# Kernel tuning notes

Hardware: AMD Instinct MI355X
Metric: run time of the kernel (lower is better)

The kernel has to match this reference:

```python
import jax, jax.numpy as jnp
import numpy as np

N_NODES = 10000
N_EDGES = 160000
MAX_K = 8
IN_NF = 64
HID = 64
ED = 16
HEADS = 4
NVEC = 5

def _mlp2_silu(x, w1, b1, w2, b2):
    # Linear -> SiLU -> Linear -> SiLU
    return jax.nn.silu(jax.nn.silu(x @ w1 + b1) @ w2 + b2)

def _mlp_out(x, w1, b1, w2, b2):
    # Linear -> SiLU -> Linear
    return jax.nn.silu(x @ w1 + b1) @ w2 + b2

def _segment_mean(data, ids, n):
    s = jax.ops.segment_sum(data, ids, num_segments=n)
    c = jax.ops.segment_sum(jnp.ones_like(data), ids, num_segments=n)
    return s / jnp.maximum(c, 1.0)

def setup_inputs() -> dict:
    key = jax.random.key(0)
    ks = jax.random.split(key, 48)
    p = lambda k, shape: jax.random.normal(k, shape, dtype=jnp.float32) * 0.05
    inp = {
        "h": jax.random.normal(ks[0], (N_NODES, IN_NF), dtype=jnp.float32),
        "coord": jax.random.normal(ks[1], (N_NODES, 3), dtype=jnp.float32),
        "edges": jax.random.randint(ks[2], (2, N_EDGES), 0, N_NODES),
        "nvecs": jax.random.normal(ks[3], (N_NODES, NVEC, 3), dtype=jnp.float32),
        "edge_attr": jax.random.normal(ks[4], (N_EDGES, ED), dtype=jnp.float32),
        "node_attr": jax.random.normal(ks[5], (N_NODES, HID), dtype=jnp.float32),
        "init_coord": jax.random.normal(ks[6], (N_NODES, 3), dtype=jnp.float32),
    }
    kidx = jax.random.randint(ks[7], (N_EDGES, 2, MAX_K), 0, N_EDGES)
    red = jax.random.uniform(ks[8], (N_EDGES, MAX_K)) < 0.2
    inp["klist"] = jnp.where(red[:, None, :], -1, kidx)
    chem_in = 2 * IN_NF + 2 * HID + ED
    pos_in = NVEC + 15 + ED  # edge_coords_nf(20) + edges_in_d
    inp.update({
        "w_chem1": p(ks[9], (chem_in, HID)), "b_chem1": jnp.zeros((HID,), jnp.float32),
        "w_chem2": p(ks[10], (HID, HID)), "b_chem2": jnp.zeros((HID,), jnp.float32),
        "w_pos1": p(ks[11], (pos_in, HID)), "b_pos1": jnp.zeros((HID,), jnp.float32),
        "w_pos2": p(ks[12], (HID, HID)), "b_pos2": jnp.zeros((HID,), jnp.float32),
        "w_sh": p(ks[13], (HID, HID)), "b_sh": jnp.zeros((HID,), jnp.float32),
        "w_att": p(ks[14], (HID, 1)), "b_att": jnp.zeros((1,), jnp.float32),
        "wq": p(ks[15], (HEADS, HID, HID)),
        "wk": p(ks[16], (HEADS, HID, HID)),
        "wv": p(ks[17], (HEADS, HID, HID)),
        "wb": p(ks[18], (HEADS, HID)),
        "wg": p(ks[19], (HEADS, HID, HID)), "bg": jnp.zeros((HEADS, HID), jnp.float32),
        "w_out": p(ks[20], (HEADS * HID, HID)), "b_out": jnp.zeros((HID,), jnp.float32),
        "wu1": p(ks[21], (HID, HID)), "bu1": jnp.zeros((HID,), jnp.float32),
        "wu2": p(ks[22], (HID, 1)), "bu2": jnp.zeros((1,), jnp.float32),
        "wx1": p(ks[23], (HID, HID)), "bx1": jnp.zeros((HID,), jnp.float32),
        "wx2": p(ks[24], (HID, 1)), "bx2": jnp.zeros((1,), jnp.float32),
        "wh1": p(ks[25], (2 * HID + IN_NF, HID)), "bh1": jnp.zeros((HID,), jnp.float32),
        "wh2": p(ks[26], (HID, HID)), "bh2": jnp.zeros((HID,), jnp.float32),
    })
    return inp

def reference(h, coord, edges, nvecs, edge_attr, node_attr, init_coord, klist,
              w_chem1, b_chem1, w_chem2, b_chem2, w_pos1, b_pos1, w_pos2, b_pos2,
              w_sh, b_sh, w_att, b_att, wq, wk, wv, wb, wg, bg, w_out, b_out,
              wu1, bu1, wu2, bu2, wx1, bx1, wx2, bx2, wh1, bh1, wh2, bh2):
    row, col = edges[0], edges[1]
    # radial features + normalized coordinate differences
    cd = coord[row] - coord[col]
    cd = cd / (jnp.linalg.norm(cd, axis=-1, keepdims=True) + 1e-8)
    init_radial = jnp.sum(cd ** 2, axis=1, keepdims=True)                 # (E, 1)
    radial = jnp.exp(init_radial * (-0.5 / 2.25 ** jnp.arange(15.0)))     # (E, 15)
    nprod = jnp.sum(nvecs[row] * nvecs[col], axis=-1)                     # (E, NVEC)
    chem = _mlp2_silu(jnp.concatenate([h[row], h[col], node_attr[row], node_attr[col], edge_attr], axis=1),
                      w_chem1, b_chem1, w_chem2, b_chem2)
    pos = _mlp2_silu(jnp.concatenate([nprod, radial, edge_attr], axis=1),
                     w_pos1, b_pos1, w_pos2, b_pos2)
    z = jax.nn.silu(chem @ w_sh + b_sh) * pos
    z = z * jax.nn.sigmoid(z @ w_att + b_att)
    # triangle k-NN attention over edges
    idx_i2k, idx_j2k = klist[:, 0], klist[:, 1]                           # (E, K)
    red = idx_i2k == -1
    heads = []
    for hd in range(HEADS):
        q = z @ wq[hd]; k_ = z @ wk[hd]; v = z @ wv[hd]; b = z @ wb[hd]
        g = jax.nn.sigmoid(z @ wg[hd] + bg[hd])
        tri_k = jnp.where(red[:, :, None], 0.0, k_[idx_i2k])              # (E, K, HID)
        tri_b = jnp.where(red, 0.0, b[idx_j2k])                           # (E, K)
        tri_v = v[idx_i2k]                                                # (E, K, HID)
        alpha = jnp.einsum('ed,ekd->ek', q, tri_k) / np.sqrt(HID) + tri_b
        alpha = jax.nn.softmax(jnp.where(red, -10000.0, alpha), axis=1)
        heads.append(g * jnp.einsum('ek,ekd->ed', alpha, tri_v))
    m = jnp.concatenate(heads, axis=-1) @ w_out + b_out
    # equivariant coordinate update
    ita = 0.2
    x_trans = cd * (_mlp_out(chem, wu1, bu1, wu2, bu2) * _mlp_out(pos, wx1, bx1, wx2, bx2))
    x_agg = _segment_mean(x_trans, row, N_NODES)
    coord_new = ita * init_coord + (1.0 - ita) * coord + x_agg
    m_agg = _segment_mean(m, row, N_NODES)
    h_new = h + _mlp_out(jnp.concatenate([h, node_attr, m_agg], axis=-1), wh1, bh1, wh2, bh2)
    return (h_new, coord_new)
```

## Files before the change

### kernel.cpp

```cpp
#include <hip/hip_runtime.h>
#include <math.h>

#define NE 160000
#define NN 10000

#define DEV __device__ __forceinline__

typedef float v2f __attribute__((ext_vector_type(2)));
typedef __attribute__((ext_vector_type(8))) short bf16x8;
typedef __attribute__((ext_vector_type(4))) float f32x4;

DEV float fsilu(float x) { return x / (1.0f + __expf(-x)); }
DEV float fsig(float x)  { return 1.0f / (1.0f + __expf(-x)); }

DEV unsigned pack2(float a, float b) {
  unsigned ua = __float_as_uint(a); ua += 0x7FFFu + ((ua >> 16) & 1u);
  unsigned ub = __float_as_uint(b); ub += 0x7FFFu + ((ub >> 16) & 1u);
  return (ua >> 16) | (ub & 0xFFFF0000u);
}

DEV unsigned packf8_4(float a, float b, float c, float d) {
  int r = __builtin_amdgcn_cvt_pk_fp8_f32(a, b, 0, false);
  r = __builtin_amdgcn_cvt_pk_fp8_f32(c, d, r, true);
  return (unsigned)r;
}
template<bool HI>
DEV v2f up2(unsigned u) { return __builtin_amdgcn_cvt_pk_f32_fp8((int)u, HI); }

DEV float dot16(uint4 u, const float* q, float d) {
  v2f f;
  f = up2<false>(u.x); d = fmaf(f.x, q[0],  d); d = fmaf(f.y, q[1],  d);
  f = up2<true >(u.x); d = fmaf(f.x, q[2],  d); d = fmaf(f.y, q[3],  d);
  f = up2<false>(u.y); d = fmaf(f.x, q[4],  d); d = fmaf(f.y, q[5],  d);
  f = up2<true >(u.y); d = fmaf(f.x, q[6],  d); d = fmaf(f.y, q[7],  d);
  f = up2<false>(u.z); d = fmaf(f.x, q[8],  d); d = fmaf(f.y, q[9],  d);
  f = up2<true >(u.z); d = fmaf(f.x, q[10], d); d = fmaf(f.y, q[11], d);
  f = up2<false>(u.w); d = fmaf(f.x, q[12], d); d = fmaf(f.y, q[13], d);
  f = up2<true >(u.w); d = fmaf(f.x, q[14], d); d = fmaf(f.y, q[15], d);
  return d;
}
DEV void acc16(uint4 u, float pk, float* o) {
  v2f f;
  f = up2<false>(u.x); o[0]  = fmaf(pk, f.x, o[0]);  o[1]  = fmaf(pk, f.y, o[1]);
  f = up2<true >(u.x); o[2]  = fmaf(pk, f.x, o[2]);  o[3]  = fmaf(pk, f.y, o[3]);
  f = up2<false>(u.y); o[4]  = fmaf(pk, f.x, o[4]);  o[5]  = fmaf(pk, f.y, o[5]);
  f = up2<true >(u.y); o[6]  = fmaf(pk, f.x, o[6]);  o[7]  = fmaf(pk, f.y, o[7]);
  f = up2<false>(u.z); o[8]  = fmaf(pk, f.x, o[8]);  o[9]  = fmaf(pk, f.y, o[9]);
  f = up2<true >(u.z); o[10] = fmaf(pk, f.x, o[10]); o[11] = fmaf(pk, f.y, o[11]);
  f = up2<false>(u.w); o[12] = fmaf(pk, f.x, o[12]); o[13] = fmaf(pk, f.y, o[13]);
  f = up2<true >(u.w); o[14] = fmaf(pk, f.x, o[14]); o[15] = fmaf(pk, f.y, o[15]);
}

DEV void ldrow16(const unsigned* __restrict__ p, unsigned (&r)[16]) {
#pragma unroll
  for (int t = 0; t < 4; ++t) {
    uint4 u = ((const uint4*)p)[t];
    r[4*t] = u.x; r[4*t+1] = u.y; r[4*t+2] = u.z; r[4*t+3] = u.w;
  }
}
DEV void unpackf8(const unsigned (&p)[16], float (&o)[64]) {
#pragma unroll
  for (int t = 0; t < 16; ++t) {
    v2f f0 = up2<false>(p[t]);
    v2f f1 = up2<true >(p[t]);
    o[4*t+0] = f0.x; o[4*t+1] = f0.y; o[4*t+2] = f1.x; o[4*t+3] = f1.y;
  }
}
DEV void store32(float* dst, const float (&a)[32]) {
#pragma unroll
  for (int j = 0; j < 32; j += 4)
    *(float4*)(dst + j) = make_float4(a[j], a[j+1], a[j+2], a[j+3]);
}

DEV bf16x8 packrow8(const float* __restrict__ p) {
  float4 a = *(const float4*)p;
  float4 b = *(const float4*)(p + 4);
  uint4 u = make_uint4(pack2(a.x, a.y), pack2(a.z, a.w),
                       pack2(b.x, b.y), pack2(b.z, b.w));
  return __builtin_bit_cast(bf16x8, u);
}

DEV void mm4(const unsigned short* __restrict__ wm, int er, int q,
             const bf16x8 (&bfr)[2], f32x4 (&acc)[4]) {
#pragma unroll
  for (int nf = 0; nf < 4; ++nf) {
    const unsigned short* ar = wm + (size_t)(nf * 16 + er) * 64 + q * 8;
    const bf16x8 a0 = *(const bf16x8*)ar;
    const bf16x8 a1 = *(const bf16x8*)(ar + 32);
    acc[nf] = __builtin_amdgcn_mfma_f32_16x16x32_bf16(a0, bfr[0], acc[nf], 0, 0, 0);
    acc[nf] = __builtin_amdgcn_mfma_f32_16x16x32_bf16(a1, bfr[1], acc[nf], 0, 0, 0);
  }
}

__global__ void __launch_bounds__(256)
k_count(const int* __restrict__ edges, int* __restrict__ icnt) {
  int e = blockIdx.x * 256 + threadIdx.x;
  if (e < NE) atomicAdd(&icnt[edges[e]], 1);
}

__global__ void __launch_bounds__(256)
k_scan(const int* __restrict__ icnt, int* __restrict__ ioffs) {
  __shared__ int part[256];
  const int t = threadIdx.x;
  const int base = t * 40;
  int loc[40];
  int s = 0;
#pragma unroll
  for (int i = 0; i < 40; ++i) {
    int idx = base + i;
    int v = (idx < NN) ? icnt[idx] : 0;
    loc[i] = v; s += v;
  }
  part[t] = s;
  __syncthreads();
  for (int off = 1; off < 256; off <<= 1) {
    int v = (t >= off) ? part[t - off] : 0;
    __syncthreads();
    part[t] += v;
    __syncthreads();
  }
  int run = (t == 0) ? 0 : part[t - 1];
#pragma unroll
  for (int i = 0; i < 40; ++i) {
    int idx = base + i;
    if (idx < NN) { ioffs[idx] = run; run += loc[i]; }
  }
  if (t == 255) ioffs[NN] = NE;
}

__global__ void __launch_bounds__(256)
k_fill(const int* __restrict__ edges, const int* __restrict__ ioffs,
       int* __restrict__ icur, int* __restrict__ eidx) {
  int e = blockIdx.x * 256 + threadIdx.x;
  if (e >= NE) return;
  int r = edges[e];
  int p = atomicAdd(&icur[r], 1);
  eidx[ioffs[r] + p] = e;
}

__global__ void __launch_bounds__(256)
k_chem1m(const float* __restrict__ h, const float* __restrict__ na,
         const float* __restrict__ ea, const int* __restrict__ edges,
         const unsigned short* __restrict__ wtb, const float* __restrict__ b1,
         float* __restrict__ act1c) {
  const int lane = threadIdx.x & 63;
  const int wid  = threadIdx.x >> 6;
  const int er   = lane & 15;
  const int q    = lane >> 4;
  const int e    = blockIdx.x * 64 + wid * 16 + er;
  const int r = edges[e], c = edges[NE + e];

  const f32x4 zero = {0.f, 0.f, 0.f, 0.f};
  f32x4 acc[4] = {zero, zero, zero, zero};
  bf16x8 f[2];
  const float* xr;
  xr = h  + (size_t)r * 64; f[0] = packrow8(xr + q * 8); f[1] = packrow8(xr + 32 + q * 8);
  mm4(wtb + (size_t)29 * 4096, er, q, f, acc);
  xr = h  + (size_t)c * 64; f[0] = packrow8(xr + q * 8); f[1] = packrow8(xr + 32 + q * 8);
  mm4(wtb + (size_t)30 * 4096, er, q, f, acc);
  xr = na + (size_t)r * 64; f[0] = packrow8(xr + q * 8); f[1] = packrow8(xr + 32 + q * 8);
  mm4(wtb + (size_t)31 * 4096, er, q, f, acc);
  xr = na + (size_t)c * 64; f[0] = packrow8(xr + q * 8); f[1] = packrow8(xr + 32 + q * 8);
  mm4(wtb + (size_t)32 * 4096, er, q, f, acc);
  {
    bf16x8 ef;
    if (q < 2) ef = packrow8(ea + (size_t)e * 16 + q * 8);
    else { uint4 z4 = make_uint4(0, 0, 0, 0); ef = __builtin_bit_cast(bf16x8, z4); }
    const unsigned short* wm = wtb + (size_t)33 * 4096;
#pragma unroll
    for (int nf = 0; nf < 4; ++nf) {
      const bf16x8 a0 = *(const bf16x8*)(wm + (size_t)(nf * 16 + er) * 64 + q * 8);
      acc[nf] = __builtin_amdgcn_mfma_f32_16x16x32_bf16(a0, ef, acc[nf], 0, 0, 0);
    }
  }
#pragma unroll
  for (int nf = 0; nf < 4; ++nf) {
    const float4 b4 = *(const float4*)(b1 + nf * 16 + q * 4);
    *(float4*)(act1c + (size_t)e * 64 + nf * 16 + q * 4) =
        make_float4(fsilu(acc[nf].x + b4.x), fsilu(acc[nf].y + b4.y),
                    fsilu(acc[nf].z + b4.z), fsilu(acc[nf].w + b4.w));
  }
}

__global__ void __launch_bounds__(256)
k_pos1(const float* __restrict__ coord, const float* __restrict__ nv,
       const float* __restrict__ ea, const int* __restrict__ edges,
       const float* __restrict__ w1, const float* __restrict__ b1,
       float* __restrict__ act1p) {
  const int e = blockIdx.x * 256 + threadIdx.x;
  const int co = blockIdx.y * 32;
  const int r = edges[e], c = edges[NE + e];

  float dx = coord[r * 3 + 0] - coord[c * 3 + 0];
  float dy = coord[r * 3 + 1] - coord[c * 3 + 1];
  float dz = coord[r * 3 + 2] - coord[c * 3 + 2];
  float nrm = sqrtf(dx * dx + dy * dy + dz * dz);
  float inv = 1.0f / (nrm + 1e-8f);
  dx *= inv; dy *= inv; dz *= inv;
  float ir = dx * dx + dy * dy + dz * dz;

  float in[36];
#pragma unroll
  for (int v = 0; v < 5; ++v) {
    float s = 0.f;
#pragma unroll
    for (int d = 0; d < 3; ++d)
      s += nv[(size_t)r * 15 + v * 3 + d] * nv[(size_t)c * 15 + v * 3 + d];
    in[v] = s;
  }
  {
    float cexp = -0.5f;
#pragma unroll
    for (int k = 0; k < 15; ++k) { in[5 + k] = __expf(ir * cexp); cexp *= (1.0f / 2.25f); }
  }
#pragma unroll
  for (int k = 0; k < 16; k += 4) {
    float4 e4 = *(const float4*)(ea + (size_t)e * 16 + k);
    in[20 + k] = e4.x; in[21 + k] = e4.y; in[22 + k] = e4.z; in[23 + k] = e4.w;
  }

  float acc[32];
#pragma unroll
  for (int j = 0; j < 32; ++j) acc[j] = b1[co + j];
#pragma unroll
  for (int k = 0; k < 36; ++k) {
    const float x = in[k];
    const float* wr = w1 + (size_t)k * 64 + co;
#pragma unroll
    for (int j = 0; j < 32; ++j) acc[j] = fmaf(x, wr[j], acc[j]);
  }
#pragma unroll
  for (int j = 0; j < 32; ++j) acc[j] = fsilu(acc[j]);
  store32(act1p + (size_t)e * 64 + co, acc);
}

__global__ void __launch_bounds__(256)
k_wprep(const float* __restrict__ wk, const float* __restrict__ wv,
        const float* __restrict__ wq, const float* __restrict__ wg,
        const float* __restrict__ wsh, const float* __restrict__ wu1,
        const float* __restrict__ wx1, const float* __restrict__ wout,
        const float* __restrict__ wh1, const float* __restrict__ wh2,
        const float* __restrict__ w2c, const float* __restrict__ w2p,
        const float* __restrict__ wc1,
        unsigned short* __restrict__ wtb) {
  const int m = blockIdx.x;
  const float* src;
  bool pad16 = false, permk = false;
  if (m < 16) {
    const int hd = m >> 2, which = m & 3;
    src = ((which == 0) ? wk : (which == 1) ? wv : (which == 2) ? wq : wg)
          + (size_t)hd * 4096;
  } else if (m < 19) {
    src = (m == 16) ? wsh : (m == 17) ? wu1 : wx1;
  } else if (m < 23) {
    src = wout + (size_t)(m - 19) * 4096;
    permk = true;
  } else if (m < 26) {
    src = wh1 + (size_t)(m - 23) * 4096;
  } else if (m == 26) {
    src = wh2;
  } else if (m == 27) {
    src = w2c;
  } else if (m == 28) {
    src = w2p;
  } else if (m < 33) {
    src = wc1 + (size_t)(m - 29) * 4096;
  } else {
    src = wc1 + (size_t)4 * 4096;
    pad16 = true;
  }
  const int t = threadIdx.x;
#pragma unroll
  for (int i = 0; i < 16; ++i) {
    int idx = t * 16 + i;
    int n = idx >> 6, kk = idx & 63;
    int kr = permk ? (((kk >> 2) & 3) * 16 + (kk >> 4) * 4 + (kk & 3)) : kk;
    float v = (pad16 && kr >= 16) ? 0.f : src[kr * 64 + n];
    unsigned u = __float_as_uint(v);
    u += 0x7FFFu + ((u >> 16) & 1u);
    wtb[(size_t)m * 4096 + idx] = (unsigned short)(u >> 16);
  }
}

__global__ void __launch_bounds__(256)
k_l2s(const float* __restrict__ coord, const int* __restrict__ edges,
      const float* __restrict__ act1c, const float* __restrict__ act1p,
      const unsigned short* __restrict__ wtb,
      const float* __restrict__ b2c, const float* __restrict__ b2p,
      const float* __restrict__ bsh,
      const float* __restrict__ watt, const float* __restrict__ batt,
      const float* __restrict__ bu1, const float* __restrict__ wu2,
      const float* __restrict__ bu2,
      const float* __restrict__ bx1, const float* __restrict__ wx2,
      const float* __restrict__ bx2,
      const float* __restrict__ wb,
      unsigned* __restrict__ zb, float* __restrict__ be,
      float* __restrict__ x_sum, float* __restrict__ cntf) {
  __shared__ float ltc[4][16][68];
  __shared__ float ltp[4][16][68];
  const int lane = threadIdx.x & 63;
  const int wid  = threadIdx.x >> 6;
  const int er   = lane & 15;
  const int q    = lane >> 4;
  const int e    = blockIdx.x * 64 + wid * 16 + er;

  const f32x4 zero = {0.f, 0.f, 0.f, 0.f};
  bf16x8 f[2];

  {
    const float* xr = act1c + (size_t)e * 64;
    f[0] = packrow8(xr + q * 8); f[1] = packrow8(xr + 32 + q * 8);
  }
  f32x4 cD[4] = {zero, zero, zero, zero};
  mm4(wtb + (size_t)27 * 4096, er, q, f, cD);
#pragma unroll
  for (int nf = 0; nf < 4; ++nf) {
    const float4 bc = *(const float4*)(b2c + nf * 16 + q * 4);
    *(float4*)&ltc[wid][er][nf * 16 + q * 4] =
        make_float4(fsilu(cD[nf].x + bc.x), fsilu(cD[nf].y + bc.y),
                    fsilu(cD[nf].z + bc.z), fsilu(cD[nf].w + bc.w));
  }
  {
    const float* xr = act1p + (size_t)e * 64;
    f[0] = packrow8(xr + q * 8); f[1] = packrow8(xr + 32 + q * 8);
  }
  f32x4 pD[4] = {zero, zero, zero, zero};
  mm4(wtb + (size_t)28 * 4096, er, q, f, pD);
  float pv[16];
#pragma unroll
  for (int nf = 0; nf < 4; ++nf) {
    const float4 bp = *(const float4*)(b2p + nf * 16 + q * 4);
    pv[4*nf+0] = fsilu(pD[nf].x + bp.x); pv[4*nf+1] = fsilu(pD[nf].y + bp.y);
    pv[4*nf+2] = fsilu(pD[nf].z + bp.z); pv[4*nf+3] = fsilu(pD[nf].w + bp.w);
    *(float4*)&ltp[wid][er][nf * 16 + q * 4] =
        make_float4(pv[4*nf+0], pv[4*nf+1], pv[4*nf+2], pv[4*nf+3]);
  }
  bf16x8 cf[2], pf[2];
  cf[0] = packrow8(&ltc[wid][er][q * 8]); cf[1] = packrow8(&ltc[wid][er][32 + q * 8]);
  pf[0] = packrow8(&ltp[wid][er][q * 8]); pf[1] = packrow8(&ltp[wid][er][32 + q * 8]);

  float z[16];
  {
    f32x4 acc[4] = {zero, zero, zero, zero};
    mm4(wtb + (size_t)16 * 4096, er, q, cf, acc);
#pragma unroll
    for (int nf = 0; nf < 4; ++nf) {
      const float4 b4 = *(const float4*)(bsh + nf * 16 + q * 4);
      z[4*nf+0] = fsilu(acc[nf].x + b4.x) * pv[4*nf+0];
      z[4*nf+1] = fsilu(acc[nf].y + b4.y) * pv[4*nf+1];
      z[4*nf+2] = fsilu(acc[nf].z + b4.z) * pv[4*nf+2];
      z[4*nf+3] = fsilu(acc[nf].w + b4.w) * pv[4*nf+3];
    }
  }
  {
    float ap = 0.f;
#pragma unroll
    for (int nf = 0; nf < 4; ++nf)
#pragma unroll
      for (int r = 0; r < 4; ++r)
        ap = fmaf(z[4*nf+r], watt[nf * 16 + q * 4 + r], ap);
    ap += __shfl_xor(ap, 16);
    ap += __shfl_xor(ap, 32);
    const float sg = fsig(ap + batt[0]);
#pragma unroll
    for (int j = 0; j < 16; ++j) z[j] *= sg;
  }
  {
    unsigned* zrow = zb + (size_t)e * 32 + q * 2;
#pragma unroll
    for (int nf = 0; nf < 4; ++nf) {
      uint2 w = make_uint2(pack2(z[4*nf+0], z[4*nf+1]), pack2(z[4*nf+2], z[4*nf+3]));
      *(uint2*)(zrow + nf * 8) = w;
    }
  }
  {
    float bb[4];
#pragma unroll
    for (int hd = 0; hd < 4; ++hd) {
      float b = 0.f;
#pragma unroll
      for (int nf = 0; nf < 4; ++nf)
#pragma unroll
        for (int r = 0; r < 4; ++r)
          b = fmaf(z[4*nf+r], wb[hd * 64 + nf * 16 + q * 4 + r], b);
      b += __shfl_xor(b, 16);
      b += __shfl_xor(b, 32);
      bb[hd] = b;
    }
    if (q == 0)
      *(float4*)(be + (size_t)e * 4) = make_float4(bb[0], bb[1], bb[2], bb[3]);
  }
  float u;
  {
    f32x4 acc[4] = {zero, zero, zero, zero};
    mm4(wtb + (size_t)17 * 4096, er, q, cf, acc);
    float up = 0.f;
#pragma unroll
    for (int nf = 0; nf < 4; ++nf) {
      const float4 b4 = *(const float4*)(bu1 + nf * 16 + q * 4);
      const float4 w4 = *(const float4*)(wu2 + nf * 16 + q * 4);
      up = fmaf(fsilu(acc[nf].x + b4.x), w4.x, up);
      up = fmaf(fsilu(acc[nf].y + b4.y), w4.y, up);
      up = fmaf(fsilu(acc[nf].z + b4.z), w4.z, up);
      up = fmaf(fsilu(acc[nf].w + b4.w), w4.w, up);
    }
    up += __shfl_xor(up, 16);
    up += __shfl_xor(up, 32);
    u = up + bu2[0];
  }
  float xs;
  {
    f32x4 acc[4] = {zero, zero, zero, zero};
    mm4(wtb + (size_t)18 * 4096, er, q, pf, acc);
    float xp = 0.f;
#pragma unroll
    for (int nf = 0; nf < 4; ++nf) {
      const float4 b4 = *(const float4*)(bx1 + nf * 16 + q * 4);
      const float4 w4 = *(const float4*)(wx2 + nf * 16 + q * 4);
      xp = fmaf(fsilu(acc[nf].x + b4.x), w4.x, xp);
      xp = fmaf(fsilu(acc[nf].y + b4.y), w4.y, xp);
      xp = fmaf(fsilu(acc[nf].z + b4.z), w4.z, xp);
      xp = fmaf(fsilu(acc[nf].w + b4.w), w4.w, xp);
    }
    xp += __shfl_xor(xp, 16);
    xp += __shfl_xor(xp, 32);
    xs = xp + bx2[0];
  }

  if (q == 0) {
    const int r = edges[e], c = edges[NE + e];
    float dx = coord[r * 3 + 0] - coord[c * 3 + 0];
    float dy = coord[r * 3 + 1] - coord[c * 3 + 1];
    float dz = coord[r * 3 + 2] - coord[c * 3 + 2];
    float nrm = sqrtf(dx * dx + dy * dy + dz * dz);
    float inv = 1.0f / (nrm + 1e-8f);
    float t = u * xs;
    atomicAdd(&x_sum[r * 3 + 0], dx * inv * t);
    atomicAdd(&x_sum[r * 3 + 1], dy * inv * t);
    atomicAdd(&x_sum[r * 3 + 2], dz * inv * t);
    atomicAdd(&cntf[r], 1.0f);
  }
}

__global__ void __launch_bounds__(256)
k_projm(const unsigned* __restrict__ zb, const unsigned short* __restrict__ wtb,
        const float* __restrict__ bg,
        unsigned* __restrict__ ksep, unsigned* __restrict__ vsep,
        unsigned* __restrict__ qho, unsigned* __restrict__ gf8) {
  const int lane = threadIdx.x & 63;
  const int wid  = threadIdx.x >> 6;
  const int er   = lane & 15;
  const int q    = lane >> 4;
  const int e0   = blockIdx.x * 128 + wid * 32 + er;

  bf16x8 zf[2][2];
#pragma unroll
  for (int et = 0; et < 2; ++et) {
    const unsigned* zrow = zb + (size_t)(e0 + et * 16) * 32;
    zf[et][0] = __builtin_bit_cast(bf16x8, *(const uint4*)(zrow + q * 4));
    zf[et][1] = __builtin_bit_cast(bf16x8, *(const uint4*)(zrow + 16 + q * 4));
  }

  const f32x4 zero = {0.f, 0.f, 0.f, 0.f};
#pragma unroll 1
  for (int m = 0; m < 16; ++m) {
    const unsigned short* wm = wtb + (size_t)m * 4096;
    f32x4 acc[2][4];
#pragma unroll
    for (int et = 0; et < 2; ++et)
#pragma unroll
      for (int nf = 0; nf < 4; ++nf) acc[et][nf] = zero;
#pragma unroll
    for (int nf = 0; nf < 4; ++nf) {
      const unsigned short* ar = wm + (size_t)(nf * 16 + er) * 64 + q * 8;
      const bf16x8 a0 = *(const bf16x8*)ar;
      const bf16x8 a1 = *(const bf16x8*)(ar + 32);
#pragma unroll
      for (int et = 0; et < 2; ++et) {
        acc[et][nf] = __builtin_amdgcn_mfma_f32_16x16x32_bf16(a0, zf[et][0], acc[et][nf], 0, 0, 0);
        acc[et][nf] = __builtin_amdgcn_mfma_f32_16x16x32_bf16(a1, zf[et][1], acc[et][nf], 0, 0, 0);
      }
    }
    const int hd = m >> 2, which = m & 3;
#pragma unroll
    for (int et = 0; et < 2; ++et) {
      const size_t rec = (size_t)(e0 + et * 16) * 4 + hd;
      unsigned* dst = (which == 0) ? (ksep + rec * 16)
                    : (which == 1) ? (vsep + rec * 16)
                    : (which == 2) ? (qho + rec * 16)
                                   : (gf8 + rec * 16);
      unsigned pk[4];
      if (which == 3) {
#pragma unroll
        for (int nf = 0; nf < 4; ++nf) {
          const float4 b4 = *(const float4*)(bg + hd * 64 + nf * 16 + q * 4);
          pk[nf] = packf8_4(fsig(acc[et][nf].x + b4.x), fsig(acc[et][nf].y + b4.y),
                            fsig(acc[et][nf].z + b4.z), fsig(acc[et][nf].w + b4.w));
        }
      } else {
#pragma unroll
        for (int nf = 0; nf < 4; ++nf)
          pk[nf] = packf8_4(acc[et][nf].x, acc[et][nf].y,
                            acc[et][nf].z, acc[et][nf].w);
      }
      *(uint4*)(dst + q * 4) = make_uint4(pk[0], pk[1], pk[2], pk[3]);
    }
  }
}

__global__ void __launch_bounds__(256)
k_attn(unsigned* __restrict__ qho, unsigned* __restrict__ gf8,
       const unsigned* __restrict__ ksep, const unsigned* __restrict__ vsep,
       const float* __restrict__ be, const int* __restrict__ klist) {
  const int t = blockIdx.x * 256 + threadIdx.x;
  const int e = t >> 2, hd = t & 3;

  float q[64];
  {
    unsigned qp[16];
    ldrow16(qho + (size_t)t * 16, qp);
    unpackf8(qp, q);
  }

  int i2[8], j2[8];
#pragma unroll
  for (int kn = 0; kn < 8; ++kn) {
    i2[kn] = klist[(size_t)e * 16 + kn];
    j2[kn] = klist[(size_t)e * 16 + 8 + kn];
  }
  float bv[8];
#pragma unroll
  for (int kn = 0; kn < 8; ++kn)
    bv[kn] = be[(size_t)((i2[kn] < 0) ? 0 : j2[kn]) * 4 + hd];

  const uint4* k4 = (const uint4*)ksep;
  float alpha[8];
#pragma unroll 2
  for (int kn = 0; kn < 8; ++kn) {
    if (i2[kn] < 0) { alpha[kn] = -10000.0f; continue; }
    const uint4* kr = k4 + ((size_t)i2[kn] * 4 + hd) * 4;
    uint4 u0 = kr[0], u1 = kr[1], u2 = kr[2], u3 = kr[3];
    float d = 0.f;
    d = dot16(u0, q,      d);
    d = dot16(u1, q + 16, d);
    d = dot16(u2, q + 32, d);
    d = dot16(u3, q + 48, d);
    alpha[kn] = d * 0.125f + bv[kn];
  }
  float mx = alpha[0];
#pragma unroll
  for (int kn = 1; kn < 8; ++kn) mx = fmaxf(mx, alpha[kn]);
  float p[8], s = 0.f;
#pragma unroll
  for (int kn = 0; kn < 8; ++kn) { p[kn] = __expf(alpha[kn] - mx); s += p[kn]; }
  float is = 1.0f / s;
#pragma unroll
  for (int kn = 0; kn < 8; ++kn) p[kn] *= is;

  float ov[64];
#pragma unroll
  for (int j = 0; j < 64; ++j) ov[j] = 0.f;
  const uint4* v4 = (const uint4*)vsep;
#pragma unroll 2
  for (int kn = 0; kn < 8; ++kn) {
    int vi = (i2[kn] < 0) ? (NE - 1) : i2[kn];
    const uint4* vr = v4 + ((size_t)vi * 4 + hd) * 4;
    uint4 u0 = vr[0], u1 = vr[1], u2 = vr[2], u3 = vr[3];
    const float pk = p[kn];
    acc16(u0, pk, ov +  0);
    acc16(u1, pk, ov + 16);
    acc16(u2, pk, ov + 32);
    acc16(u3, pk, ov + 48);
  }
  {
    unsigned gp[16];
    ldrow16(gf8 + (size_t)t * 16, gp);
    float g[64];
    unpackf8(gp, g);
#pragma unroll
    for (int j = 0; j < 64; ++j) ov[j] *= g[j];
  }
  {
    unsigned* qr = qho + (size_t)t * 16;
    unsigned* gr = gf8 + (size_t)t * 16;
#pragma unroll
    for (int t2 = 0; t2 < 2; ++t2) {
      ((uint4*)qr)[t2] = make_uint4(pack2(ov[8*t2+0],  ov[8*t2+1]),  pack2(ov[8*t2+2],  ov[8*t2+3]),
                                    pack2(ov[8*t2+4],  ov[8*t2+5]),  pack2(ov[8*t2+6],  ov[8*t2+7]));
      ((uint4*)qr)[2+t2] = make_uint4(pack2(ov[16+8*t2+0], ov[16+8*t2+1]), pack2(ov[16+8*t2+2], ov[16+8*t2+3]),
                                      pack2(ov[16+8*t2+4], ov[16+8*t2+5]), pack2(ov[16+8*t2+6], ov[16+8*t2+7]));
      ((uint4*)gr)[t2] = make_uint4(pack2(ov[32+8*t2+0], ov[32+8*t2+1]), pack2(ov[32+8*t2+2], ov[32+8*t2+3]),
                                    pack2(ov[32+8*t2+4], ov[32+8*t2+5]), pack2(ov[32+8*t2+6], ov[32+8*t2+7]));
      ((uint4*)gr)[2+t2] = make_uint4(pack2(ov[48+8*t2+0], ov[48+8*t2+1]), pack2(ov[48+8*t2+2], ov[48+8*t2+3]),
                                      pack2(ov[48+8*t2+4], ov[48+8*t2+5]), pack2(ov[48+8*t2+6], ov[48+8*t2+7]));
    }
  }
}

__global__ void __launch_bounds__(256)
k_mout(const unsigned* __restrict__ qho, const unsigned* __restrict__ gf8,
       const unsigned short* __restrict__ wtb, float* __restrict__ medge) {
  const int lane = threadIdx.x & 63;
  const int wid  = threadIdx.x >> 6;
  const int er   = lane & 15;
  const int q    = lane >> 4;
  const int e0   = blockIdx.x * 256 + wid * 64 + er;

  const f32x4 zero = {0.f, 0.f, 0.f, 0.f};
  f32x4 acc[4][4];
#pragma unroll
  for (int et = 0; et < 4; ++et)
#pragma unroll
    for (int nf = 0; nf < 4; ++nf) acc[et][nf] = zero;

#pragma unroll 1
  for (int hd = 0; hd < 4; ++hd) {
    const unsigned short* wm = wtb + (size_t)(19 + hd) * 4096;
    bf16x8 hf[4][2];
#pragma unroll
    for (int et = 0; et < 4; ++et) {
      const size_t rec = (size_t)(e0 + et * 16) * 4 + hd;
      hf[et][0] = __builtin_bit_cast(bf16x8, *(const uint4*)(qho + rec * 16 + q * 4));
      hf[et][1] = __builtin_bit_cast(bf16x8, *(const uint4*)(gf8 + rec * 16 + q * 4));
    }
#pragma unroll
    for (int nf = 0; nf < 4; ++nf) {
      const unsigned short* ar = wm + (size_t)(nf * 16 + er) * 64 + q * 8;
      const bf16x8 a0 = *(const bf16x8*)ar;
      const bf16x8 a1 = *(const bf16x8*)(ar + 32);
#pragma unroll
      for (int et = 0; et < 4; ++et) {
        acc[et][nf] = __builtin_amdgcn_mfma_f32_16x16x32_bf16(a0, hf[et][0], acc[et][nf], 0, 0, 0);
        acc[et][nf] = __builtin_amdgcn_mfma_f32_16x16x32_bf16(a1, hf[et][1], acc[et][nf], 0, 0, 0);
      }
    }
  }
#pragma unroll
  for (int et = 0; et < 4; ++et)
#pragma unroll
    for (int nf = 0; nf < 4; ++nf)
      *(float4*)(medge + (size_t)(e0 + et * 16) * 64 + nf * 16 + q * 4) =
          make_float4(acc[et][nf].x, acc[et][nf].y, acc[et][nf].z, acc[et][nf].w);
}

__global__ void __launch_bounds__(256)
k_nodesum(const float* __restrict__ medge, const int* __restrict__ ioffs,
          const int* __restrict__ eidx, float* __restrict__ m_sum) {
  const int wid = threadIdx.x >> 6, lane = threadIdx.x & 63;
  const int n = blockIdx.x * 4 + wid;
  if (n >= NN) return;
  const int beg = ioffs[n], end = ioffs[n + 1];
  float acc = 0.f;
  for (int i = beg; i < end; ++i) {
    int e = eidx[i];
    acc += medge[(size_t)e * 64 + lane];
  }
  m_sum[(size_t)n * 64 + lane] = acc;
}

__global__ void __launch_bounds__(256)
k_finm(const float* __restrict__ h, const float* __restrict__ na,
       const float* __restrict__ coord, const float* __restrict__ icoord,
       const float* __restrict__ m_sum, const float* __restrict__ x_sum,
       const float* __restrict__ cntf, const float* __restrict__ bout,
       const unsigned short* __restrict__ wtb,
       const float* __restrict__ bh1, const float* __restrict__ bh2,
       float* __restrict__ out) {
  __shared__ float lt[4][16][68];
  const int lane = threadIdx.x & 63;
  const int wid  = threadIdx.x >> 6;
  const int er   = lane & 15;
  const int q    = lane >> 4;
  const int e    = blockIdx.x * 64 + wid * 16 + er;
  const bool valid = e < NN;
  const int el = valid ? e : 0;

  const float* hr = h + (size_t)el * 64;
  const float* nr = na + (size_t)el * 64;
  const float* mr = m_sum + (size_t)el * 64;
  const float cn = cntf[el];
  const float invc = 1.0f / fmaxf(cn, 1.0f);
  const float bsc = (cn > 0.f) ? 1.0f : 0.0f;

  bf16x8 hf[2], naf[2], mf[2];
  hf[0]  = packrow8(hr + q * 8); hf[1]  = packrow8(hr + 32 + q * 8);
  naf[0] = packrow8(nr + q * 8); naf[1] = packrow8(nr + 32 + q * 8);
#pragma unroll
  for (int half = 0; half < 2; ++half) {
    const int o = half * 32 + q * 8;
    const float4 m0 = *(const float4*)(mr + o);
    const float4 m1 = *(const float4*)(mr + o + 4);
    const float4 b0 = *(const float4*)(bout + o);
    const float4 b1 = *(const float4*)(bout + o + 4);
    float ma[8];
    ma[0] = fmaf(m0.x, invc, b0.x * bsc); ma[1] = fmaf(m0.y, invc, b0.y * bsc);
    ma[2] = fmaf(m0.z, invc, b0.z * bsc); ma[3] = fmaf(m0.w, invc, b0.w * bsc);
    ma[4] = fmaf(m1.x, invc, b1.x * bsc); ma[5] = fmaf(m1.y, invc, b1.y * bsc);
    ma[6] = fmaf(m1.z, invc, b1.z * bsc); ma[7] = fmaf(m1.w, invc, b1.w * bsc);
    uint4 u = make_uint4(pack2(ma[0], ma[1]), pack2(ma[2], ma[3]),
                         pack2(ma[4], ma[5]), pack2(ma[6], ma[7]));
    mf[half] = __builtin_bit_cast(bf16x8, u);
  }

  const f32x4 zero = {0.f, 0.f, 0.f, 0.f};
  f32x4 acc[4] = {zero, zero, zero, zero};
  mm4(wtb + (size_t)23 * 4096, er, q, hf,  acc);
  mm4(wtb + (size_t)24 * 4096, er, q, naf, acc);
  mm4(wtb + (size_t)25 * 4096, er, q, mf,  acc);
#pragma unroll
  for (int nf = 0; nf < 4; ++nf) {
    const float4 b4 = *(const float4*)(bh1 + nf * 16 + q * 4);
    float* d = &lt[wid][er][nf * 16 + q * 4];
    d[0] = fsilu(acc[nf].x + b4.x); d[1] = fsilu(acc[nf].y + b4.y);
    d[2] = fsilu(acc[nf].z + b4.z); d[3] = fsilu(acc[nf].w + b4.w);
  }
  __syncthreads();
  bf16x8 sf[2];
  sf[0] = packrow8(&lt[wid][er][q * 8]);
  sf[1] = packrow8(&lt[wid][er][32 + q * 8]);
  f32x4 a2[4] = {zero, zero, zero, zero};
  mm4(wtb + (size_t)26 * 4096, er, q, sf, a2);
  if (valid) {
#pragma unroll
    for (int nf = 0; nf < 4; ++nf) {
      const float4 b4 = *(const float4*)(bh2 + nf * 16 + q * 4);
      const float4 h4 = *(const float4*)(hr + nf * 16 + q * 4);
      *(float4*)(out + (size_t)e * 64 + nf * 16 + q * 4) =
          make_float4(a2[nf].x + b4.x + h4.x, a2[nf].y + b4.y + h4.y,
                      a2[nf].z + b4.z + h4.z, a2[nf].w + b4.w + h4.w);
    }
    if (q == 0) {
#pragma unroll
      for (int d = 0; d < 3; ++d)
        out[(size_t)NN * 64 + e * 3 + d] =
            0.2f * icoord[e * 3 + d] + 0.8f * coord[e * 3 + d] + x_sum[e * 3 + d] * invc;
    }
  }
}

extern "C" void kernel_launch(void* const* d_in, const int* in_sizes, int n_in,
                              void* d_out, int out_size, void* d_ws, size_t ws_size,
                              hipStream_t stream) {
  (void)in_sizes; (void)n_in; (void)out_size; (void)ws_size;
  const float* h      = (const float*)d_in[0];
  const float* coord  = (const float*)d_in[1];
  const int*   edges  = (const int*)  d_in[2];
  const float* nvecs  = (const float*)d_in[3];
  const float* ea     = (const float*)d_in[4];
  const float* na     = (const float*)d_in[5];
  const float* icoord = (const float*)d_in[6];
  const int*   klist  = (const int*)  d_in[7];
  const float* w_chem1 = (const float*)d_in[8];
  const float* b_chem1 = (const float*)d_in[9];
  const float* w_chem2 = (const float*)d_in[10];
  const float* b_chem2 = (const float*)d_in[11];
  const float* w_pos1  = (const float*)d_in[12];
  const float* b_pos1  = (const float*)d_in[13];
  const float* w_pos2  = (const float*)d_in[14];
  const float* b_pos2  = (const float*)d_in[15];
  const float* w_sh    = (const float*)d_in[16];
  const float* b_sh    = (const float*)d_in[17];
  const float* w_att   = (const float*)d_in[18];
  const float* b_att   = (const float*)d_in[19];
  const float* wq      = (const float*)d_in[20];
  const float* wk      = (const float*)d_in[21];
  const float* wv      = (const float*)d_in[22];
  const float* wb      = (const float*)d_in[23];
  const float* wg      = (const float*)d_in[24];
  const float* bg      = (const float*)d_in[25];
  const float* w_out   = (const float*)d_in[26];
  const float* b_out   = (const float*)d_in[27];
  const float* wu1     = (const float*)d_in[28];
  const float* bu1     = (const float*)d_in[29];
  const float* wu2     = (const float*)d_in[30];
  const float* bu2     = (const float*)d_in[31];
  const float* wx1     = (const float*)d_in[32];
  const float* bx1     = (const float*)d_in[33];
  const float* wx2     = (const float*)d_in[34];
  const float* bx2     = (const float*)d_in[35];
  const float* wh1     = (const float*)d_in[36];
  const float* bh1     = (const float*)d_in[37];
  const float* wh2     = (const float*)d_in[38];
  const float* bh2     = (const float*)d_in[39];

  float* out = (float*)d_out;
  float* ws  = (float*)d_ws;
  float* R1 = ws;
  float* R2 = R1 + (size_t)NE * 64;
  float* R3 = R2 + (size_t)NE * 64;
  float* R4 = R3 + (size_t)NE * 64;
  float* zbf   = R4 + (size_t)NE * 64;
  float* x_sum = zbf + (size_t)NE * 32;
  float* cntf  = x_sum + (size_t)NN * 3;
  int*   icnt  = (int*)(cntf + NN);
  int*   icur  = icnt + NN;
  float* m_sum = (float*)(icur + NN);
  float* be    = m_sum + (size_t)NN * 64;
  unsigned short* wtb = (unsigned short*)(be + (size_t)4 * NE);
  int*   ioffs = (int*)(wtb + 34 * 4096);
  int*   eidx  = ioffs + (NN + 1);

  unsigned* ksep = (unsigned*)R1;
  unsigned* vsep = (unsigned*)R2;
  unsigned* qho  = (unsigned*)R3;
  unsigned* gf8  = (unsigned*)R4;
  unsigned* zb   = (unsigned*)zbf;
  float* medge = R1;

  (void)hipMemsetAsync(x_sum, 0, ((size_t)NN * 3 + NN + NN + NN) * sizeof(float), stream);

  dim3 b256(256);
  dim3 gflat(NE / 256);

  k_wprep<<<dim3(34), b256, 0, stream>>>(wk, wv, wq, wg, w_sh, wu1, wx1, w_out,
                                         wh1, wh2, w_chem2, w_pos2, w_chem1, wtb);
  k_count<<<gflat, b256, 0, stream>>>(edges, icnt);
  k_scan <<<dim3(1), b256, 0, stream>>>(icnt, ioffs);
  k_fill <<<gflat, b256, 0, stream>>>(edges, ioffs, icur, eidx);

  k_chem1m<<<dim3(NE / 64), b256, 0, stream>>>(h, na, ea, edges, wtb, b_chem1, R1);
  k_pos1  <<<dim3(NE / 256, 2), b256, 0, stream>>>(coord, nvecs, ea, edges, w_pos1, b_pos1, R2);
  k_l2s   <<<dim3(NE / 64), b256, 0, stream>>>(coord, edges, R1, R2, wtb,
                                               b_chem2, b_pos2, b_sh, w_att, b_att,
                                               bu1, wu2, bu2, bx1, wx2, bx2, wb,
                                               zb, be, x_sum, cntf);
  k_projm<<<dim3(NE / 128), b256, 0, stream>>>(zb, wtb, bg, ksep, vsep, qho, gf8);
  k_attn <<<dim3(NE * 4 / 256), b256, 0, stream>>>(qho, gf8, ksep, vsep, be, klist);
  k_mout <<<dim3(NE / 256), b256, 0, stream>>>(qho, gf8, wtb, medge);
  k_nodesum<<<dim3((NN + 3) / 4), b256, 0, stream>>>(medge, ioffs, eidx, m_sum);
  k_finm<<<dim3((NN + 63) / 64), b256, 0, stream>>>(h, na, coord, icoord, m_sum, x_sum,
                                                    cntf, b_out, wtb, bh1, bh2, out);
}
```

Before: 641.8 us.

## Fuse attention with output projection via LDS-staged bf16 head outputs

Merges the attention kernel and the output-projection MFMA kernel into one. Each thread packs its gated head output to bf16 in shared memory, and after a barrier each wave runs MFMAs over the four heads to write edge messages straight to global memory. This removes the global round trip of per-head outputs and one kernel launch. The edge-message buffer now aliases the query region. The cost is a 33 KB LDS tile per block, which may limit occupancy, plus smaller MFMA tiles per wave.

```diff
diff --git a/kernel.cpp b/kernel.cpp
--- a/kernel.cpp
+++ b/kernel.cpp
@@ -509,10 +509,13 @@
 }
 
 __global__ void __launch_bounds__(256)
-k_attn(unsigned* __restrict__ qho, unsigned* __restrict__ gf8,
-       const unsigned* __restrict__ ksep, const unsigned* __restrict__ vsep,
-       const float* __restrict__ be, const int* __restrict__ klist) {
-  const int t = blockIdx.x * 256 + threadIdx.x;
+k_attnm(const unsigned* __restrict__ qho, const unsigned* __restrict__ gf8,
+        const unsigned* __restrict__ ksep, const unsigned* __restrict__ vsep,
+        const float* __restrict__ be, const int* __restrict__ klist,
+        const unsigned short* __restrict__ wtb, float* __restrict__ medge) {
+  __shared__ unsigned hlds[256][33];
+  const int tid = threadIdx.x;
+  const int t = blockIdx.x * 256 + tid;
   const int e = t >> 2, hd = t & 3;
 
   float q[64];
@@ -579,68 +582,40 @@
     unpackf8(gp, g);
 #pragma unroll
     for (int j = 0; j < 64; ++j) ov[j] *= g[j];
-  }
-  {
-    unsigned* qr = qho + (size_t)t * 16;
-    unsigned* gr = gf8 + (size_t)t * 16;
-#pragma unroll
-    for (int t2 = 0; t2 < 2; ++t2) {
-      ((uint4*)qr)[t2] = make_uint4(pack2(ov[8*t2+0],  ov[8*t2+1]),  pack2(ov[8*t2+2],  ov[8*t2+3]),
-                                    pack2(ov[8*t2+4],  ov[8*t2+5]),  pack2(ov[8*t2+6],  ov[8*t2+7]));
-      ((uint4*)qr)[2+t2] = make_uint4(pack2(ov[16+8*t2+0], ov[16+8*t2+1]), pack2(ov[16+8*t2+2], ov[16+8*t2+3]),
-                                      pack2(ov[16+8*t2+4], ov[16+8*t2+5]), pack2(ov[16+8*t2+6], ov[16+8*t2+7]));
-      ((uint4*)gr)[t2] = make_uint4(pack2(ov[32+8*t2+0], ov[32+8*t2+1]), pack2(ov[32+8*t2+2], ov[32+8*t2+3]),
-                                    pack2(ov[32+8*t2+4], ov[32+8*t2+5]), pack2(ov[32+8*t2+6], ov[32+8*t2+7]));
-      ((uint4*)gr)[2+t2] = make_uint4(pack2(ov[48+8*t2+0], ov[48+8*t2+1]), pack2(ov[48+8*t2+2], ov[48+8*t2+3]),
-                                      pack2(ov[48+8*t2+4], ov[48+8*t2+5]), pack2(ov[48+8*t2+6], ov[48+8*t2+7]));
-    }
-  }
-}
-
-__global__ void __launch_bounds__(256)
-k_mout(const unsigned* __restrict__ qho, const unsigned* __restrict__ gf8,
-       const unsigned short* __restrict__ wtb, float* __restrict__ medge) {
-  const int lane = threadIdx.x & 63;
-  const int wid  = threadIdx.x >> 6;
+#pragma unroll
+    for (int j = 0; j < 32; ++j) hlds[tid][j] = pack2(ov[2*j], ov[2*j+1]);
+  }
+  __syncthreads();
+
+  const int lane = tid & 63;
+  const int w    = tid >> 6;
   const int er   = lane & 15;
-  const int q    = lane >> 4;
-  const int e0   = blockIdx.x * 256 + wid * 64 + er;
+  const int qq   = lane >> 4;
+  const int eg   = blockIdx.x * 64 + w * 16 + er;
 
   const f32x4 zero = {0.f, 0.f, 0.f, 0.f};
-  f32x4 acc[4][4];
-#pragma unroll
-  for (int et = 0; et < 4; ++et)
-#pragma unroll
-    for (int nf = 0; nf < 4; ++nf) acc[et][nf] = zero;
-
+  f32x4 acc[4] = {zero, zero, zero, zero};
 #pragma unroll 1
-  for (int hd = 0; hd < 4; ++hd) {
-    const unsigned short* wm = wtb + (size_t)(19 + hd) * 4096;
-    bf16x8 hf[4][2];
-#pragma unroll
-    for (int et = 0; et < 4; ++et) {
-      const size_t rec = (size_t)(e0 + et * 16) * 4 + hd;
-      hf[et][0] = __builtin_bit_cast(bf16x8, *(const uint4*)(qho + rec * 16 + q * 4));
-      hf[et][1] = __builtin_bit_cast(bf16x8, *(const uint4*)(gf8 + rec * 16 + q * 4));
-    }
+  for (int hd2 = 0; hd2 < 4; ++hd2) {
+    const unsigned* hr = hlds[(w * 16 + er) * 4 + hd2];
+    uint4 u0 = make_uint4(hr[qq*4], hr[qq*4+1], hr[qq*4+2], hr[qq*4+3]);
+    uint4 u1 = make_uint4(hr[16+qq*4], hr[16+qq*4+1], hr[16+qq*4+2], hr[16+qq*4+3]);
+    const bf16x8 hf0 = __builtin_bit_cast(bf16x8, u0);
+    const bf16x8 hf1 = __builtin_bit_cast(bf16x8, u1);
+    const unsigned short* wm = wtb + (size_t)(19 + hd2) * 4096;
 #pragma unroll
     for (int nf = 0; nf < 4; ++nf) {
-      const unsigned short* ar = wm + (size_t)(nf * 16 + er) * 64 + q * 8;
+      const unsigned short* ar = wm + (size_t)(nf * 16 + er) * 64 + qq * 8;
       const bf16x8 a0 = *(const bf16x8*)ar;
       const bf16x8 a1 = *(const bf16x8*)(ar + 32);
-#pragma unroll
-      for (int et = 0; et < 4; ++et) {
-        acc[et][nf] = __builtin_amdgcn_mfma_f32_16x16x32_bf16(a0, hf[et][0], acc[et][nf], 0, 0, 0);
-        acc[et][nf] = __builtin_amdgcn_mfma_f32_16x16x32_bf16(a1, hf[et][1], acc[et][nf], 0, 0, 0);
-      }
-    }
-  }
-#pragma unroll
-  for (int et = 0; et < 4; ++et)
-#pragma unroll
-    for (int nf = 0; nf < 4; ++nf)
-      *(float4*)(medge + (size_t)(e0 + et * 16) * 64 + nf * 16 + q * 4) =
-          make_float4(acc[et][nf].x, acc[et][nf].y, acc[et][nf].z, acc[et][nf].w);
+      acc[nf] = __builtin_amdgcn_mfma_f32_16x16x32_bf16(a0, hf0, acc[nf], 0, 0, 0);
+      acc[nf] = __builtin_amdgcn_mfma_f32_16x16x32_bf16(a1, hf1, acc[nf], 0, 0, 0);
+    }
+  }
+#pragma unroll
+  for (int nf = 0; nf < 4; ++nf)
+    *(float4*)(medge + (size_t)eg * 64 + nf * 16 + qq * 4) =
+        make_float4(acc[nf].x, acc[nf].y, acc[nf].z, acc[nf].w);
 }
 
 __global__ void __launch_bounds__(256)
@@ -805,7 +780,7 @@
   unsigned* qho  = (unsigned*)R3;
   unsigned* gf8  = (unsigned*)R4;
   unsigned* zb   = (unsigned*)zbf;
-  float* medge = R1;
+  float* medge = R3;
 
   (void)hipMemsetAsync(x_sum, 0, ((size_t)NN * 3 + NN + NN + NN) * sizeof(float), stream);
 
@@ -825,8 +800,8 @@
                                                bu1, wu2, bu2, bx1, wx2, bx2, wb,
                                                zb, be, x_sum, cntf);
   k_projm<<<dim3(NE / 128), b256, 0, stream>>>(zb, wtb, bg, ksep, vsep, qho, gf8);
-  k_attn <<<dim3(NE * 4 / 256), b256, 0, stream>>>(qho, gf8, ksep, vsep, be, klist);
-  k_mout <<<dim3(NE / 256), b256, 0, stream>>>(qho, gf8, wtb, medge);
+  k_attnm<<<dim3(NE * 4 / 256), b256, 0, stream>>>(qho, gf8, ksep, vsep, be, klist,
+                                                   wtb, medge);
   k_nodesum<<<dim3((NN + 3) / 4), b256, 0, stream>>>(medge, ioffs, eidx, m_sum);
   k_finm<<<dim3((NN + 63) / 64), b256, 0, stream>>>(h, na, coord, icoord, m_sum, x_sum,
                                                     cntf, b_out, wtb, bh1, bh2, out);
```

Measured after the change: 629.6 us. About the same (-1.9%).
